# Kernel tuning notes

Measured on AMD Instinct MI355X. Metric: run time of the kernel, lower is better.

The kernel has to match this reference:

```python
import jax, jax.numpy as jnp
import numpy as np

D_MODEL = 1024
HEAD = 64

def setup_inputs() -> dict:
    key = jax.random.key(0)
    ks = jax.random.split(key, 7)
    s = 1.0 / np.sqrt(D_MODEL)
    x = jax.random.normal(ks[0], (4, 2048, D_MODEL), dtype=jnp.float32)
    Wq = jax.random.uniform(ks[1], (D_MODEL, HEAD), jnp.float32, -s, s)
    bq = jax.random.uniform(ks[2], (HEAD,), jnp.float32, -s, s)
    Wk = jax.random.uniform(ks[3], (D_MODEL, HEAD), jnp.float32, -s, s)
    bk = jax.random.uniform(ks[4], (HEAD,), jnp.float32, -s, s)
    Wv = jax.random.uniform(ks[5], (D_MODEL, HEAD), jnp.float32, -s, s)
    bv = jax.random.uniform(ks[6], (HEAD,), jnp.float32, -s, s)
    return {"x": x, "Wq": Wq, "bq": bq, "Wk": Wk, "bk": bk, "Wv": Wv, "bv": bv}

def reference(x, Wq, bq, Wk, bk, Wv, bv):
    # x: [b, s, d]
    q = x @ Wq + bq  # [b, s, h]
    k = x @ Wk + bk
    v = x @ Wv + bv
    scale = 1.0 / jnp.sqrt(jnp.asarray(HEAD, x.dtype))
    scores = jnp.einsum('bqh,bkh->bqk', q, k) * scale  # [b, s, s]
    seq_len = x.shape[1]
    mask = jnp.triu(jnp.ones((seq_len, seq_len), dtype=bool), k=1)
    scores = jnp.where(mask, -jnp.inf, scores)
    attn = jax.nn.softmax(scores, axis=-1)
    return jnp.einsum('bqk,bkh->bqh', attn, v)
```

## Files before the change

kernel.cpp:

```cpp
#include <hip/hip_runtime.h>
#include <hip/hip_bf16.h>

#define D_MODEL 1024
#define HEAD    64
#define SEQ     2048
#define BATCH   4
#define ROWS    (BATCH * SEQ)

typedef __attribute__((ext_vector_type(8))) short  short8;
typedef __attribute__((ext_vector_type(4))) short  short4v;
typedef __attribute__((ext_vector_type(4))) float  f32x4;

__device__ __forceinline__ unsigned short f2bf(float f) {
    union { __hip_bfloat16 h; unsigned short u; } c;
    c.h = __float2bfloat16(f);
    return c.u;
}

__global__ __launch_bounds__(256) void conv_w(
    const float* __restrict__ Wq, const float* __restrict__ Wk,
    const float* __restrict__ Wv, unsigned short* __restrict__ Wt)
{
    __shared__ float Lw[64][65];
    const int tid = threadIdx.x;
    const int mat = blockIdx.x >> 4;
    const int k0  = (blockIdx.x & 15) * 64;
    const float* W = (mat == 0) ? Wq : (mat == 1 ? Wk : Wv);

    #pragma unroll
    for (int j = 0; j < 4; ++j) {
        const int idx = j * 1024 + tid * 4;
        const int r = idx >> 6, c = idx & 63;
        f32x4 v4 = *(const f32x4*)(W + (size_t)(k0 + r) * HEAD + c);
        Lw[r][c] = v4[0]; Lw[r][c+1] = v4[1]; Lw[r][c+2] = v4[2]; Lw[r][c+3] = v4[3];
    }
    __syncthreads();

    const int col = tid >> 2, kc = (tid & 3) * 16;
    short8 o0, o1;
    #pragma unroll
    for (int j = 0; j < 8; ++j) o0[j] = f2bf(Lw[kc + j][col]);
    #pragma unroll
    for (int j = 0; j < 8; ++j) o1[j] = f2bf(Lw[kc + 8 + j][col]);
    unsigned short* dst = Wt + (size_t)(mat * 64 + col) * D_MODEL + k0 + kc;
    *(short8*)(dst)     = o0;
    *(short8*)(dst + 8) = o1;
}

__global__ __launch_bounds__(256) void gemm_qkv(
    const float* __restrict__ x, const unsigned short* __restrict__ Wt,
    const float* __restrict__ bq, const float* __restrict__ bk,
    const float* __restrict__ bv,
    unsigned short* __restrict__ qb, unsigned short* __restrict__ kb,
    unsigned short* __restrict__ vt)
{
    __shared__ unsigned short Xs[16 * 1032];
    __shared__ float Vx[16][66];

    const int tid  = threadIdx.x;
    const int lane = tid & 63;
    const int w    = tid >> 6;
    const int l15  = lane & 15;
    const int g    = lane >> 4;
    const int row0 = blockIdx.x * 16;

    {
        const int xrow  = tid >> 4;
        const int cbase = (tid & 15) * 4;
        #pragma unroll
        for (int j = 0; j < 16; ++j) {
            const int col = j * 64 + cbase;
            f32x4 v4 = *(const f32x4*)(x + (size_t)(row0 + xrow) * D_MODEL + col);
            short4v pk;
            pk[0] = f2bf(v4[0]); pk[1] = f2bf(v4[1]);
            pk[2] = f2bf(v4[2]); pk[3] = f2bf(v4[3]);
            *(short4v*)&Xs[xrow * 1032 + col] = pk;
        }
    }
    __syncthreads();

    f32x4 acc[3] = {};
    const size_t wrow0 = (size_t)(w * 48 + l15) * D_MODEL;

    short8 bA[3][2], bB[3][2];
    #pragma unroll
    for (int ni = 0; ni < 3; ++ni) {
        bA[ni][0] = *(const short8*)(Wt + wrow0 + (size_t)ni * 16 * D_MODEL + g * 8);
        bA[ni][1] = *(const short8*)(Wt + wrow0 + (size_t)ni * 16 * D_MODEL + 32 + g * 8);
    }

    auto gbody = [&](int t, short8 (&bcur)[3][2], short8 (&bnxt)[3][2]) {
        const int k0 = t * 64;
        if (t + 1 < 16) {
            #pragma unroll
            for (int ni = 0; ni < 3; ++ni) {
                const size_t base = wrow0 + (size_t)ni * 16 * D_MODEL + k0 + 64;
                bnxt[ni][0] = *(const short8*)(Wt + base + g * 8);
                bnxt[ni][1] = *(const short8*)(Wt + base + 32 + g * 8);
            }
        }
        short8 af0 = *(const short8*)&Xs[l15 * 1032 + k0 + g * 8];
        short8 af1 = *(const short8*)&Xs[l15 * 1032 + k0 + 32 + g * 8];
        #pragma unroll
        for (int ni = 0; ni < 3; ++ni) {
            acc[ni] = __builtin_amdgcn_mfma_f32_16x16x32_bf16(af0, bcur[ni][0], acc[ni], 0, 0, 0);
            acc[ni] = __builtin_amdgcn_mfma_f32_16x16x32_bf16(af1, bcur[ni][1], acc[ni], 0, 0, 0);
        }
    };

    #pragma unroll 1
    for (int t = 0; t < 16; t += 2) {
        gbody(t,     bA, bB);
        gbody(t + 1, bB, bA);
    }

    #pragma unroll
    for (int ni = 0; ni < 3; ++ni) {
        const int col = w * 48 + ni * 16 + l15;
        const int mat = col >> 6, mc = col & 63;
        const float bias = (mat == 0 ? bq : (mat == 1 ? bk : bv))[mc];
        #pragma unroll
        for (int r = 0; r < 4; ++r) {
            const int rl = g * 4 + r;
            const float val = acc[ni][r] + bias;
            if (mat == 0)      qb[(size_t)(row0 + rl) * HEAD + mc] = f2bf(val * 0.125f);
            else if (mat == 1) kb[(size_t)(row0 + rl) * HEAD + mc] = f2bf(val);
            else               Vx[rl][mc] = val;
        }
    }
    __syncthreads();

    {
        const int d = tid >> 2, kvc = (tid & 3) * 4;
        short4v o;
        #pragma unroll
        for (int j = 0; j < 4; ++j) o[j] = f2bf(Vx[kvc + j][d]);
        const int bb = row0 >> 11, kvloc = row0 & 2047;
        *(short4v*)(vt + ((size_t)bb * HEAD + d) * SEQ + kvloc + kvc) = o;
    }
}

__global__ __launch_bounds__(512) void attn_fwd(
    const unsigned short* __restrict__ qb, const unsigned short* __restrict__ kb,
    const unsigned short* __restrict__ vt, float* __restrict__ out)
{
    __shared__ unsigned short Qs[16 * 68];
    __shared__ unsigned short Ps[8][16 * 40];
    __shared__ float Cs[8][16 * 68];
    __shared__ float Sm[128], Sl[128];

    const int tid  = threadIdx.x;
    const int lane = tid & 63;
    const int w    = tid >> 6;
    const int l15  = lane & 15;
    const int g    = lane >> 4;
    const int b    = blockIdx.y;
    const int p    = blockIdx.x;

    const unsigned short* qg = qb + (size_t)b * SEQ * HEAD;
    const unsigned short* kg = kb + (size_t)b * SEQ * HEAD;
    const unsigned short* vg = vt + (size_t)b * HEAD * SEQ;

    #pragma unroll 1
    for (int half = 0; half < 2; ++half) {
        const int j     = half ? (127 - p) : p;
        const int q0    = j * 16;
        const int iters = (q0 + 16 + 255) >> 8;

        if (tid < 128) {
            const int row = tid >> 3, slot = tid & 7;
            *(short8*)&Qs[row * 68 + slot * 8] =
                *(const short8*)(qg + (size_t)(q0 + row) * HEAD + slot * 8);
        }
        __syncthreads();

        const short8 qf0 = *(const short8*)&Qs[l15 * 68 + g * 8];
        const short8 qf1 = *(const short8*)&Qs[l15 * 68 + 32 + g * 8];

        float m_w = -1.0e30f, l_w = 0.0f;
        f32x4 acc[4] = {};

        short8 kA[4], kB2[4];
        #pragma unroll
        for (int u = 0; u < 4; ++u) {
            const int f = u >> 1, ks = u & 1;
            kA[u] = *(const short8*)(
                kg + (size_t)(w * 32 + f * 16 + l15) * HEAD + ks * 32 + g * 8);
        }

        auto body = [&](int it, short8 (&kcur)[4], short8 (&knxt)[4]) {
            const int kv0 = it * 256;

            short8 vc0, vc1, vc2, vc3;
            {
                const size_t vb = (size_t)l15 * SEQ + kv0 + w * 32 + g * 8;
                vc0 = *(const short8*)(vg + vb);
                vc1 = *(const short8*)(vg + vb + (size_t)16 * SEQ);
                vc2 = *(const short8*)(vg + vb + (size_t)32 * SEQ);
                vc3 = *(const short8*)(vg + vb + (size_t)48 * SEQ);
            }

            if (it + 1 < iters) {
                #pragma unroll
                for (int u = 0; u < 4; ++u) {
                    const int f = u >> 1, ks = u & 1;
                    knxt[u] = *(const short8*)(
                        kg + (size_t)(kv0 + 256 + w * 32 + f * 16 + l15) * HEAD
                           + ks * 32 + g * 8);
                }
            }

            f32x4 sA[2] = {};
            sA[0] = __builtin_amdgcn_mfma_f32_16x16x32_bf16(kcur[0], qf0, sA[0], 0, 0, 0);
            sA[0] = __builtin_amdgcn_mfma_f32_16x16x32_bf16(kcur[1], qf1, sA[0], 0, 0, 0);
            sA[1] = __builtin_amdgcn_mfma_f32_16x16x32_bf16(kcur[2], qf0, sA[1], 0, 0, 0);
            sA[1] = __builtin_amdgcn_mfma_f32_16x16x32_bf16(kcur[3], qf1, sA[1], 0, 0, 0);

            if (it == iters - 1) {
                const int kvb = kv0 + w * 32 + g * 4;
                const int qq  = q0 + l15;
                #pragma unroll
                for (int f = 0; f < 2; ++f)
                    #pragma unroll
                    for (int r = 0; r < 4; ++r)
                        if (kvb + f * 16 + r > qq) sA[f][r] = -1.0e30f;
            }

            float smax = sA[0][0];
            #pragma unroll
            for (int r = 1; r < 4; ++r) smax = fmaxf(smax, sA[0][r]);
            #pragma unroll
            for (int r = 0; r < 4; ++r) smax = fmaxf(smax, sA[1][r]);
            smax = fmaxf(smax, __shfl_xor(smax, 16));
            smax = fmaxf(smax, __shfl_xor(smax, 32));

            const float mnew = fmaxf(m_w, smax);
            const float corr = __expf(m_w - mnew);
            float pv[8], psum = 0.0f;
            #pragma unroll
            for (int f = 0; f < 2; ++f)
                #pragma unroll
                for (int r = 0; r < 4; ++r) {
                    pv[f * 4 + r] = __expf(sA[f][r] - mnew);
                    psum += pv[f * 4 + r];
                }
            psum += __shfl_xor(psum, 16);
            psum += __shfl_xor(psum, 32);
            l_w = l_w * corr + psum;
            m_w = mnew;

            #pragma unroll
            for (int f = 0; f < 2; ++f) {
                short4v pk;
                pk[0] = f2bf(pv[f*4+0]); pk[1] = f2bf(pv[f*4+1]);
                pk[2] = f2bf(pv[f*4+2]); pk[3] = f2bf(pv[f*4+3]);
                *(short4v*)&Ps[w][l15 * 40 + f * 16 + g * 4] = pk;
            }

            float cf[4];
            #pragma unroll
            for (int r = 0; r < 4; ++r) cf[r] = __shfl(corr, g * 4 + r);
            #pragma unroll
            for (int ni = 0; ni < 4; ++ni)
                #pragma unroll
                for (int r = 0; r < 4; ++r) acc[ni][r] *= cf[r];

            const short8 pf = *(const short8*)&Ps[w][l15 * 40 + g * 8];
            acc[0] = __builtin_amdgcn_mfma_f32_16x16x32_bf16(pf, vc0, acc[0], 0, 0, 0);
            acc[1] = __builtin_amdgcn_mfma_f32_16x16x32_bf16(pf, vc1, acc[1], 0, 0, 0);
            acc[2] = __builtin_amdgcn_mfma_f32_16x16x32_bf16(pf, vc2, acc[2], 0, 0, 0);
            acc[3] = __builtin_amdgcn_mfma_f32_16x16x32_bf16(pf, vc3, acc[3], 0, 0, 0);
        };

        #pragma unroll 1
        for (int itp = 0; itp < iters; itp += 2) {
            body(itp, kA, kB2);
            if (itp + 1 < iters) body(itp + 1, kB2, kA);
        }

        if (lane < 16) { Sm[w * 16 + lane] = m_w; Sl[w * 16 + lane] = l_w; }
        #pragma unroll
        for (int ni = 0; ni < 4; ++ni)
            #pragma unroll
            for (int r = 0; r < 4; ++r)
                Cs[w][(g * 4 + r) * 68 + ni * 16 + l15] = acc[ni][r];
        __syncthreads();

        if (tid < 256) {
            const int q = tid >> 4, d4 = (tid & 15) * 4;
            float mg = Sm[q];
            #pragma unroll
            for (int ww = 1; ww < 8; ++ww) mg = fmaxf(mg, Sm[ww * 16 + q]);
            f32x4 o = {0.f, 0.f, 0.f, 0.f};
            float lt = 0.0f;
            #pragma unroll
            for (int ww = 0; ww < 8; ++ww) {
                const float f = __expf(Sm[ww * 16 + q] - mg);
                lt += Sl[ww * 16 + q] * f;
                f32x4 c4 = *(const f32x4*)&Cs[ww][q * 68 + d4];
                o[0] += c4[0] * f; o[1] += c4[1] * f;
                o[2] += c4[2] * f; o[3] += c4[3] * f;
            }
            const float inv = 1.0f / lt;
            f32x4 res = {o[0]*inv, o[1]*inv, o[2]*inv, o[3]*inv};
            *(f32x4*)(out + ((size_t)b * SEQ + q0 + q) * HEAD + d4) = res;
        }
        __syncthreads();
    }
}

extern "C" void kernel_launch(void* const* d_in, const int* in_sizes, int n_in,
                              void* d_out, int out_size, void* d_ws, size_t ws_size,
                              hipStream_t stream) {
    const float* x  = (const float*)d_in[0];
    const float* Wq = (const float*)d_in[1];
    const float* bq = (const float*)d_in[2];
    const float* Wk = (const float*)d_in[3];
    const float* bk = (const float*)d_in[4];
    const float* Wv = (const float*)d_in[5];
    const float* bv = (const float*)d_in[6];

    unsigned short* Wt  = (unsigned short*)d_ws;
    unsigned short* qbp = Wt + (size_t)192 * D_MODEL;
    unsigned short* kbp = qbp + (size_t)ROWS * HEAD;
    unsigned short* vtp = kbp + (size_t)ROWS * HEAD;
    float* o = (float*)d_out;

    conv_w  <<<dim3(48),     dim3(256), 0, stream>>>(Wq, Wk, Wv, Wt);
    gemm_qkv<<<dim3(512),    dim3(256), 0, stream>>>(x, Wt, bq, bk, bv, qbp, kbp, vtp);
    attn_fwd<<<dim3(64, 4),  dim3(512), 0, stream>>>(qbp, kbp, vtp, o);
}
```

Measured before the change: 129.6 us.

## Fuse weight conversion, QKV GEMM and attention into one cooperative kernel

Replaces the three separate launches with a single cooperative kernel of 256 blocks of 512 threads that uses grid-wide syncs between the weight-conversion, QKV projection and attention phases, with shared memory reused through a union. The QKV GEMM now gives each block 32 rows across 8 waves, and the attention loop double-buffers V loads alongside K prefetches. The aim is to remove launch gaps and tail effects between kernels. The cost is grid.sync overhead and only 256 blocks for the GEMM phase.

```diff
diff --git a/kernel.cpp b/kernel.cpp
--- a/kernel.cpp
+++ b/kernel.cpp
@@ -1,5 +1,8 @@
 #include <hip/hip_runtime.h>
 #include <hip/hip_bf16.h>
+#include <hip/hip_cooperative_groups.h>
+
+namespace cg = cooperative_groups;
 
 #define D_MODEL 1024
 #define HEAD    64
@@ -17,54 +20,60 @@
     return c.u;
 }
 
-__global__ __launch_bounds__(256) void conv_w(
-    const float* __restrict__ Wq, const float* __restrict__ Wk,
-    const float* __restrict__ Wv, unsigned short* __restrict__ Wt)
+__global__ __launch_bounds__(512, 2) void fused_all(
+    const float* __restrict__ x,
+    const float* __restrict__ Wq, const float* __restrict__ bq,
+    const float* __restrict__ Wk, const float* __restrict__ bk,
+    const float* __restrict__ Wv, const float* __restrict__ bv,
+    unsigned short* __restrict__ Wt,
+    unsigned short* __restrict__ qb, unsigned short* __restrict__ kb,
+    unsigned short* __restrict__ vt, float* __restrict__ out)
 {
-    __shared__ float Lw[64][65];
-    const int tid = threadIdx.x;
-    const int mat = blockIdx.x >> 4;
-    const int k0  = (blockIdx.x & 15) * 64;
-    const float* W = (mat == 0) ? Wq : (mat == 1 ? Wk : Wv);
-
-    #pragma unroll
-    for (int j = 0; j < 4; ++j) {
-        const int idx = j * 1024 + tid * 4;
-        const int r = idx >> 6, c = idx & 63;
-        f32x4 v4 = *(const f32x4*)(W + (size_t)(k0 + r) * HEAD + c);
-        Lw[r][c] = v4[0]; Lw[r][c+1] = v4[1]; Lw[r][c+2] = v4[2]; Lw[r][c+3] = v4[3];
-    }
-    __syncthreads();
-
-    const int col = tid >> 2, kc = (tid & 3) * 16;
-    short8 o0, o1;
-    #pragma unroll
-    for (int j = 0; j < 8; ++j) o0[j] = f2bf(Lw[kc + j][col]);
-    #pragma unroll
-    for (int j = 0; j < 8; ++j) o1[j] = f2bf(Lw[kc + 8 + j][col]);
-    unsigned short* dst = Wt + (size_t)(mat * 64 + col) * D_MODEL + k0 + kc;
-    *(short8*)(dst)     = o0;
-    *(short8*)(dst + 8) = o1;
-}
-
-__global__ __launch_bounds__(256) void gemm_qkv(
-    const float* __restrict__ x, const unsigned short* __restrict__ Wt,
-    const float* __restrict__ bq, const float* __restrict__ bk,
-    const float* __restrict__ bv,
-    unsigned short* __restrict__ qb, unsigned short* __restrict__ kb,
-    unsigned short* __restrict__ vt)
-{
-    __shared__ unsigned short Xs[16 * 1032];
-    __shared__ float Vx[16][66];
+    __shared__ union SMem {
+        struct { float Lw[64][65]; } a;
+        struct { unsigned short Xs[32 * 1032];
+                 float Vx[32][66]; } bp;
+        struct { unsigned short Qs[16 * 68];
+                 unsigned short Ps[8][16 * 40];
+                 float Cs[8][16 * 68];
+                 float Sm[128], Sl[128]; } c;
+    } sm;
+
+    cg::grid_group grid = cg::this_grid();
 
     const int tid  = threadIdx.x;
+    const int bx   = blockIdx.x;
     const int lane = tid & 63;
     const int w    = tid >> 6;
     const int l15  = lane & 15;
     const int g    = lane >> 4;
-    const int row0 = blockIdx.x * 16;
+
+    if (bx < 48) {
+        const int mat = bx >> 4;
+        const int k0  = (bx & 15) * 64;
+        const float* W = (mat == 0) ? Wq : (mat == 1 ? Wk : Wv);
+        #pragma unroll
+        for (int j = 0; j < 2; ++j) {
+            const int idx = j * 2048 + tid * 4;
+            const int r = idx >> 6, cc = idx & 63;
+            f32x4 v4 = *(const f32x4*)(W + (size_t)(k0 + r) * HEAD + cc);
+            sm.a.Lw[r][cc]   = v4[0]; sm.a.Lw[r][cc+1] = v4[1];
+            sm.a.Lw[r][cc+2] = v4[2]; sm.a.Lw[r][cc+3] = v4[3];
+        }
+        __syncthreads();
+        const int col = tid >> 3, kc = (tid & 7) * 8;
+        short8 o;
+        #pragma unroll
+        for (int j = 0; j < 8; ++j) o[j] = f2bf(sm.a.Lw[kc + j][col]);
+        *(short8*)(Wt + (size_t)(mat * 64 + col) * D_MODEL + k0 + kc) = o;
+    }
+
+    grid.sync();
 
     {
+        const int wr = w & 1, wc = w >> 1;
+        const int row0 = bx * 32;
+
         const int xrow  = tid >> 4;
         const int cbase = (tid & 15) * 4;
         #pragma unroll
@@ -74,238 +83,224 @@
             short4v pk;
             pk[0] = f2bf(v4[0]); pk[1] = f2bf(v4[1]);
             pk[2] = f2bf(v4[2]); pk[3] = f2bf(v4[3]);
-            *(short4v*)&Xs[xrow * 1032 + col] = pk;
+            *(short4v*)&sm.bp.Xs[xrow * 1032 + col] = pk;
+        }
+        __syncthreads();
+
+        f32x4 acc[3] = {};
+        const size_t wrow0 = (size_t)(wc * 48 + l15) * D_MODEL;
+
+        short8 bA[3][2], bB[3][2];
+        #pragma unroll
+        for (int ni = 0; ni < 3; ++ni) {
+            const size_t base = wrow0 + (size_t)ni * 16 * D_MODEL;
+            bA[ni][0] = *(const short8*)(Wt + base + g * 8);
+            bA[ni][1] = *(const short8*)(Wt + base + 32 + g * 8);
+        }
+
+        auto gbody = [&](int t, short8 (&bcur)[3][2], short8 (&bnxt)[3][2]) {
+            const int k0 = t * 64;
+            if (t + 1 < 16) {
+                #pragma unroll
+                for (int ni = 0; ni < 3; ++ni) {
+                    const size_t base = wrow0 + (size_t)ni * 16 * D_MODEL + k0 + 64;
+                    bnxt[ni][0] = *(const short8*)(Wt + base + g * 8);
+                    bnxt[ni][1] = *(const short8*)(Wt + base + 32 + g * 8);
+                }
+            }
+            short8 af0 = *(const short8*)&sm.bp.Xs[(wr * 16 + l15) * 1032 + k0 + g * 8];
+            short8 af1 = *(const short8*)&sm.bp.Xs[(wr * 16 + l15) * 1032 + k0 + 32 + g * 8];
+            #pragma unroll
+            for (int ni = 0; ni < 3; ++ni) {
+                acc[ni] = __builtin_amdgcn_mfma_f32_16x16x32_bf16(af0, bcur[ni][0], acc[ni], 0, 0, 0);
+                acc[ni] = __builtin_amdgcn_mfma_f32_16x16x32_bf16(af1, bcur[ni][1], acc[ni], 0, 0, 0);
+            }
+        };
+
+        #pragma unroll 1
+        for (int t = 0; t < 16; t += 2) {
+            gbody(t,     bA, bB);
+            gbody(t + 1, bB, bA);
+        }
+
+        #pragma unroll
+        for (int ni = 0; ni < 3; ++ni) {
+            const int col = wc * 48 + ni * 16 + l15;
+            const int mat = col >> 6, mc = col & 63;
+            const float bias = (mat == 0 ? bq : (mat == 1 ? bk : bv))[mc];
+            #pragma unroll
+            for (int r = 0; r < 4; ++r) {
+                const int rl = wr * 16 + g * 4 + r;
+                const float val = acc[ni][r] + bias;
+                if (mat == 0)      qb[(size_t)(row0 + rl) * HEAD + mc] = f2bf(val * 0.125f);
+                else if (mat == 1) kb[(size_t)(row0 + rl) * HEAD + mc] = f2bf(val);
+                else               sm.bp.Vx[rl][mc] = val;
+            }
+        }
+        __syncthreads();
+
+        {
+            const int d = tid >> 3, kvc = (tid & 7) * 4;
+            short4v o;
+            #pragma unroll
+            for (int j = 0; j < 4; ++j) o[j] = f2bf(sm.bp.Vx[kvc + j][d]);
+            const int bb = row0 >> 11, kvloc = row0 & 2047;
+            *(short4v*)(vt + ((size_t)bb * HEAD + d) * SEQ + kvloc + kvc) = o;
         }
     }
-    __syncthreads();
-
-    f32x4 acc[3] = {};
-    const size_t wrow0 = (size_t)(w * 48 + l15) * D_MODEL;
-
-    short8 bA[3][2], bB[3][2];
-    #pragma unroll
-    for (int ni = 0; ni < 3; ++ni) {
-        bA[ni][0] = *(const short8*)(Wt + wrow0 + (size_t)ni * 16 * D_MODEL + g * 8);
-        bA[ni][1] = *(const short8*)(Wt + wrow0 + (size_t)ni * 16 * D_MODEL + 32 + g * 8);
-    }
-
-    auto gbody = [&](int t, short8 (&bcur)[3][2], short8 (&bnxt)[3][2]) {
-        const int k0 = t * 64;
-        if (t + 1 < 16) {
-            #pragma unroll
-            for (int ni = 0; ni < 3; ++ni) {
-                const size_t base = wrow0 + (size_t)ni * 16 * D_MODEL + k0 + 64;
-                bnxt[ni][0] = *(const short8*)(Wt + base + g * 8);
-                bnxt[ni][1] = *(const short8*)(Wt + base + 32 + g * 8);
-            }
-        }
-        short8 af0 = *(const short8*)&Xs[l15 * 1032 + k0 + g * 8];
-        short8 af1 = *(const short8*)&Xs[l15 * 1032 + k0 + 32 + g * 8];
-        #pragma unroll
-        for (int ni = 0; ni < 3; ++ni) {
-            acc[ni] = __builtin_amdgcn_mfma_f32_16x16x32_bf16(af0, bcur[ni][0], acc[ni], 0, 0, 0);
-            acc[ni] = __builtin_amdgcn_mfma_f32_16x16x32_bf16(af1, bcur[ni][1], acc[ni], 0, 0, 0);
-        }
-    };
-
-    #pragma unroll 1
-    for (int t = 0; t < 16; t += 2) {
-        gbody(t,     bA, bB);
-        gbody(t + 1, bB, bA);
-    }
-
-    #pragma unroll
-    for (int ni = 0; ni < 3; ++ni) {
-        const int col = w * 48 + ni * 16 + l15;
-        const int mat = col >> 6, mc = col & 63;
-        const float bias = (mat == 0 ? bq : (mat == 1 ? bk : bv))[mc];
-        #pragma unroll
-        for (int r = 0; r < 4; ++r) {
-            const int rl = g * 4 + r;
-            const float val = acc[ni][r] + bias;
-            if (mat == 0)      qb[(size_t)(row0 + rl) * HEAD + mc] = f2bf(val * 0.125f);
-            else if (mat == 1) kb[(size_t)(row0 + rl) * HEAD + mc] = f2bf(val);
-            else               Vx[rl][mc] = val;
-        }
-    }
-    __syncthreads();
+
+    grid.sync();
 
     {
-        const int d = tid >> 2, kvc = (tid & 3) * 4;
-        short4v o;
-        #pragma unroll
-        for (int j = 0; j < 4; ++j) o[j] = f2bf(Vx[kvc + j][d]);
-        const int bb = row0 >> 11, kvloc = row0 & 2047;
-        *(short4v*)(vt + ((size_t)bb * HEAD + d) * SEQ + kvloc + kvc) = o;
-    }
-}
-
-__global__ __launch_bounds__(512) void attn_fwd(
-    const unsigned short* __restrict__ qb, const unsigned short* __restrict__ kb,
-    const unsigned short* __restrict__ vt, float* __restrict__ out)
-{
-    __shared__ unsigned short Qs[16 * 68];
-    __shared__ unsigned short Ps[8][16 * 40];
-    __shared__ float Cs[8][16 * 68];
-    __shared__ float Sm[128], Sl[128];
-
-    const int tid  = threadIdx.x;
-    const int lane = tid & 63;
-    const int w    = tid >> 6;
-    const int l15  = lane & 15;
-    const int g    = lane >> 4;
-    const int b    = blockIdx.y;
-    const int p    = blockIdx.x;
-
-    const unsigned short* qg = qb + (size_t)b * SEQ * HEAD;
-    const unsigned short* kg = kb + (size_t)b * SEQ * HEAD;
-    const unsigned short* vg = vt + (size_t)b * HEAD * SEQ;
-
-    #pragma unroll 1
-    for (int half = 0; half < 2; ++half) {
-        const int j     = half ? (127 - p) : p;
-        const int q0    = j * 16;
-        const int iters = (q0 + 16 + 255) >> 8;
-
-        if (tid < 128) {
-            const int row = tid >> 3, slot = tid & 7;
-            *(short8*)&Qs[row * 68 + slot * 8] =
-                *(const short8*)(qg + (size_t)(q0 + row) * HEAD + slot * 8);
-        }
-        __syncthreads();
-
-        const short8 qf0 = *(const short8*)&Qs[l15 * 68 + g * 8];
-        const short8 qf1 = *(const short8*)&Qs[l15 * 68 + 32 + g * 8];
-
-        float m_w = -1.0e30f, l_w = 0.0f;
-        f32x4 acc[4] = {};
-
-        short8 kA[4], kB2[4];
-        #pragma unroll
-        for (int u = 0; u < 4; ++u) {
-            const int f = u >> 1, ks = u & 1;
-            kA[u] = *(const short8*)(
-                kg + (size_t)(w * 32 + f * 16 + l15) * HEAD + ks * 32 + g * 8);
-        }
-
-        auto body = [&](int it, short8 (&kcur)[4], short8 (&knxt)[4]) {
-            const int kv0 = it * 256;
-
-            short8 vc0, vc1, vc2, vc3;
-            {
-                const size_t vb = (size_t)l15 * SEQ + kv0 + w * 32 + g * 8;
-                vc0 = *(const short8*)(vg + vb);
-                vc1 = *(const short8*)(vg + vb + (size_t)16 * SEQ);
-                vc2 = *(const short8*)(vg + vb + (size_t)32 * SEQ);
-                vc3 = *(const short8*)(vg + vb + (size_t)48 * SEQ);
-            }
-
-            if (it + 1 < iters) {
-                #pragma unroll
-                for (int u = 0; u < 4; ++u) {
-                    const int f = u >> 1, ks = u & 1;
-                    knxt[u] = *(const short8*)(
-                        kg + (size_t)(kv0 + 256 + w * 32 + f * 16 + l15) * HEAD
-                           + ks * 32 + g * 8);
-                }
-            }
-
-            f32x4 sA[2] = {};
-            sA[0] = __builtin_amdgcn_mfma_f32_16x16x32_bf16(kcur[0], qf0, sA[0], 0, 0, 0);
-            sA[0] = __builtin_amdgcn_mfma_f32_16x16x32_bf16(kcur[1], qf1, sA[0], 0, 0, 0);
-            sA[1] = __builtin_amdgcn_mfma_f32_16x16x32_bf16(kcur[2], qf0, sA[1], 0, 0, 0);
-            sA[1] = __builtin_amdgcn_mfma_f32_16x16x32_bf16(kcur[3], qf1, sA[1], 0, 0, 0);
-
-            if (it == iters - 1) {
-                const int kvb = kv0 + w * 32 + g * 4;
-                const int qq  = q0 + l15;
+        const int b = bx >> 6;
+        const int p = bx & 63;
+
+        const unsigned short* qg = qb + (size_t)b * SEQ * HEAD;
+        const unsigned short* kg = kb + (size_t)b * SEQ * HEAD;
+        const unsigned short* vg = vt + (size_t)b * HEAD * SEQ;
+
+        #pragma unroll 1
+        for (int half = 0; half < 2; ++half) {
+            const int j     = half ? (127 - p) : p;
+            const int q0    = j * 16;
+            const int iters = (q0 + 16 + 255) >> 8;
+
+            if (tid < 128) {
+                const int row = tid >> 3, slot = tid & 7;
+                *(short8*)&sm.c.Qs[row * 68 + slot * 8] =
+                    *(const short8*)(qg + (size_t)(q0 + row) * HEAD + slot * 8);
+            }
+            __syncthreads();
+
+            const short8 qf0 = *(const short8*)&sm.c.Qs[l15 * 68 + g * 8];
+            const short8 qf1 = *(const short8*)&sm.c.Qs[l15 * 68 + 32 + g * 8];
+
+            float m_w = -1.0e30f, l_w = 0.0f;
+            f32x4 acc[4] = {};
+
+            short8 kA[4], kB2[4], vA[4], vB[4];
+            #pragma unroll
+            for (int u = 0; u < 4; ++u) {
+                const int f = u >> 1, ks = u & 1;
+                kA[u] = *(const short8*)(
+                    kg + (size_t)(w * 32 + f * 16 + l15) * HEAD + ks * 32 + g * 8);
+                vA[u] = *(const short8*)(
+                    vg + (size_t)(u * 16 + l15) * SEQ + w * 32 + g * 8);
+            }
+
+            auto body = [&](int it, short8 (&kcur)[4], short8 (&knxt)[4],
+                                    short8 (&vcur)[4], short8 (&vnxt)[4]) {
+                const int kv0 = it * 256;
+
+                if (it + 1 < iters) {
+                    #pragma unroll
+                    for (int u = 0; u < 4; ++u) {
+                        const int f = u >> 1, ks = u & 1;
+                        knxt[u] = *(const short8*)(
+                            kg + (size_t)(kv0 + 256 + w * 32 + f * 16 + l15) * HEAD
+                               + ks * 32 + g * 8);
+                        vnxt[u] = *(const short8*)(
+                            vg + (size_t)(u * 16 + l15) * SEQ + kv0 + 256 + w * 32 + g * 8);
+                    }
+                }
+
+                f32x4 sA[2] = {};
+                sA[0] = __builtin_amdgcn_mfma_f32_16x16x32_bf16(kcur[0], qf0, sA[0], 0, 0, 0);
+                sA[0] = __builtin_amdgcn_mfma_f32_16x16x32_bf16(kcur[1], qf1, sA[0], 0, 0, 0);
+                sA[1] = __builtin_amdgcn_mfma_f32_16x16x32_bf16(kcur[2], qf0, sA[1], 0, 0, 0);
+                sA[1] = __builtin_amdgcn_mfma_f32_16x16x32_bf16(kcur[3], qf1, sA[1], 0, 0, 0);
+
+                if (it == iters - 1) {
+                    const int kvb = kv0 + w * 32 + g * 4;
+                    const int qq  = q0 + l15;
+                    #pragma unroll
+                    for (int f = 0; f < 2; ++f)
+                        #pragma unroll
+                        for (int r = 0; r < 4; ++r)
+                            if (kvb + f * 16 + r > qq) sA[f][r] = -1.0e30f;
+                }
+
+                float smax = sA[0][0];
+                #pragma unroll
+                for (int r = 1; r < 4; ++r) smax = fmaxf(smax, sA[0][r]);
+                #pragma unroll
+                for (int r = 0; r < 4; ++r) smax = fmaxf(smax, sA[1][r]);
+                smax = fmaxf(smax, __shfl_xor(smax, 16));
+                smax = fmaxf(smax, __shfl_xor(smax, 32));
+
+                const float mnew = fmaxf(m_w, smax);
+                const float corr = __expf(m_w - mnew);
+                float pv[8], psum = 0.0f;
                 #pragma unroll
                 for (int f = 0; f < 2; ++f)
                     #pragma unroll
-                    for (int r = 0; r < 4; ++r)
-                        if (kvb + f * 16 + r > qq) sA[f][r] = -1.0e30f;
-            }
-
-            float smax = sA[0][0];
-            #pragma unroll
-            for (int r = 1; r < 4; ++r) smax = fmaxf(smax, sA[0][r]);
-            #pragma unroll
-            for (int r = 0; r < 4; ++r) smax = fmaxf(smax, sA[1][r]);
-            smax = fmaxf(smax, __shfl_xor(smax, 16));
-            smax = fmaxf(smax, __shfl_xor(smax, 32));
-
-            const float mnew = fmaxf(m_w, smax);
-            const float corr = __expf(m_w - mnew);
-            float pv[8], psum = 0.0f;
-            #pragma unroll
-            for (int f = 0; f < 2; ++f)
-                #pragma unroll
-                for (int r = 0; r < 4; ++r) {
-                    pv[f * 4 + r] = __expf(sA[f][r] - mnew);
-                    psum += pv[f * 4 + r];
-                }
-            psum += __shfl_xor(psum, 16);
-            psum += __shfl_xor(psum, 32);
-            l_w = l_w * corr + psum;
-            m_w = mnew;
-
-            #pragma unroll
-            for (int f = 0; f < 2; ++f) {
-                short4v pk;
-                pk[0] = f2bf(pv[f*4+0]); pk[1] = f2bf(pv[f*4+1]);
-                pk[2] = f2bf(pv[f*4+2]); pk[3] = f2bf(pv[f*4+3]);
-                *(short4v*)&Ps[w][l15 * 40 + f * 16 + g * 4] = pk;
-            }
-
-            float cf[4];
-            #pragma unroll
-            for (int r = 0; r < 4; ++r) cf[r] = __shfl(corr, g * 4 + r);
+                    for (int r = 0; r < 4; ++r) {
+                        pv[f * 4 + r] = __expf(sA[f][r] - mnew);
+                        psum += pv[f * 4 + r];
+                    }
+                psum += __shfl_xor(psum, 16);
+                psum += __shfl_xor(psum, 32);
+                l_w = l_w * corr + psum;
+                m_w = mnew;
+
+                #pragma unroll
+                for (int f = 0; f < 2; ++f) {
+                    short4v pk;
+                    pk[0] = f2bf(pv[f*4+0]); pk[1] = f2bf(pv[f*4+1]);
+                    pk[2] = f2bf(pv[f*4+2]); pk[3] = f2bf(pv[f*4+3]);
+                    *(short4v*)&sm.c.Ps[w][l15 * 40 + f * 16 + g * 4] = pk;
+                }
+
+                float cf[4];
+                #pragma unroll
+                for (int r = 0; r < 4; ++r) cf[r] = __shfl(corr, g * 4 + r);
+                #pragma unroll
+                for (int ni = 0; ni < 4; ++ni)
+                    #pragma unroll
+                    for (int r = 0; r < 4; ++r) acc[ni][r] *= cf[r];
+
+                const short8 pf = *(const short8*)&sm.c.Ps[w][l15 * 40 + g * 8];
+                acc[0] = __builtin_amdgcn_mfma_f32_16x16x32_bf16(pf, vcur[0], acc[0], 0, 0, 0);
+                acc[1] = __builtin_amdgcn_mfma_f32_16x16x32_bf16(pf, vcur[1], acc[1], 0, 0, 0);
+                acc[2] = __builtin_amdgcn_mfma_f32_16x16x32_bf16(pf, vcur[2], acc[2], 0, 0, 0);
+                acc[3] = __builtin_amdgcn_mfma_f32_16x16x32_bf16(pf, vcur[3], acc[3], 0, 0, 0);
+            };
+
+            #pragma unroll 1
+            for (int itp = 0; itp < iters; itp += 2) {
+                body(itp, kA, kB2, vA, vB);
+                if (itp + 1 < iters) body(itp + 1, kB2, kA, vB, vA);
+            }
+
+            if (lane < 16) { sm.c.Sm[w * 16 + lane] = m_w; sm.c.Sl[w * 16 + lane] = l_w; }
             #pragma unroll
             for (int ni = 0; ni < 4; ++ni)
                 #pragma unroll
-                for (int r = 0; r < 4; ++r) acc[ni][r] *= cf[r];
-
-            const short8 pf = *(const short8*)&Ps[w][l15 * 40 + g * 8];
-            acc[0] = __builtin_amdgcn_mfma_f32_16x16x32_bf16(pf, vc0, acc[0], 0, 0, 0);
-            acc[1] = __builtin_amdgcn_mfma_f32_16x16x32_bf16(pf, vc1, acc[1], 0, 0, 0);
-            acc[2] = __builtin_amdgcn_mfma_f32_16x16x32_bf16(pf, vc2, acc[2], 0, 0, 0);
-            acc[3] = __builtin_amdgcn_mfma_f32_16x16x32_bf16(pf, vc3, acc[3], 0, 0, 0);
-        };
-
-        #pragma unroll 1
-        for (int itp = 0; itp < iters; itp += 2) {
-            body(itp, kA, kB2);
-            if (itp + 1 < iters) body(itp + 1, kB2, kA);
-        }
-
-        if (lane < 16) { Sm[w * 16 + lane] = m_w; Sl[w * 16 + lane] = l_w; }
-        #pragma unroll
-        for (int ni = 0; ni < 4; ++ni)
-            #pragma unroll
-            for (int r = 0; r < 4; ++r)
-                Cs[w][(g * 4 + r) * 68 + ni * 16 + l15] = acc[ni][r];
-        __syncthreads();
-
-        if (tid < 256) {
-            const int q = tid >> 4, d4 = (tid & 15) * 4;
-            float mg = Sm[q];
-            #pragma unroll
-            for (int ww = 1; ww < 8; ++ww) mg = fmaxf(mg, Sm[ww * 16 + q]);
-            f32x4 o = {0.f, 0.f, 0.f, 0.f};
-            float lt = 0.0f;
-            #pragma unroll
-            for (int ww = 0; ww < 8; ++ww) {
-                const float f = __expf(Sm[ww * 16 + q] - mg);
-                lt += Sl[ww * 16 + q] * f;
-                f32x4 c4 = *(const f32x4*)&Cs[ww][q * 68 + d4];
-                o[0] += c4[0] * f; o[1] += c4[1] * f;
-                o[2] += c4[2] * f; o[3] += c4[3] * f;
-            }
-            const float inv = 1.0f / lt;
-            f32x4 res = {o[0]*inv, o[1]*inv, o[2]*inv, o[3]*inv};
-            *(f32x4*)(out + ((size_t)b * SEQ + q0 + q) * HEAD + d4) = res;
-        }
-        __syncthreads();
+                for (int r = 0; r < 4; ++r)
+                    sm.c.Cs[w][(g * 4 + r) * 68 + ni * 16 + l15] = acc[ni][r];
+            __syncthreads();
+
+            if (tid < 256) {
+                const int q = tid >> 4, d4 = (tid & 15) * 4;
+                float mg = sm.c.Sm[q];
+                #pragma unroll
+                for (int ww = 1; ww < 8; ++ww) mg = fmaxf(mg, sm.c.Sm[ww * 16 + q]);
+                f32x4 o = {0.f, 0.f, 0.f, 0.f};
+                float lt = 0.0f;
+                #pragma unroll
+                for (int ww = 0; ww < 8; ++ww) {
+                    const float f = __expf(sm.c.Sm[ww * 16 + q] - mg);
+                    lt += sm.c.Sl[ww * 16 + q] * f;
+                    f32x4 c4 = *(const f32x4*)&sm.c.Cs[ww][q * 68 + d4];
+                    o[0] += c4[0] * f; o[1] += c4[1] * f;
+                    o[2] += c4[2] * f; o[3] += c4[3] * f;
+                }
+                const float inv = 1.0f / lt;
+                f32x4 res = {o[0]*inv, o[1]*inv, o[2]*inv, o[3]*inv};
+                *(f32x4*)(out + ((size_t)b * SEQ + q0 + q) * HEAD + d4) = res;
+            }
+            __syncthreads();
+        }
     }
 }
 
@@ -326,7 +321,9 @@
     unsigned short* vtp = kbp + (size_t)ROWS * HEAD;
     float* o = (float*)d_out;
 
-    conv_w  <<<dim3(48),     dim3(256), 0, stream>>>(Wq, Wk, Wv, Wt);
-    gemm_qkv<<<dim3(512),    dim3(256), 0, stream>>>(x, Wt, bq, bk, bv, qbp, kbp, vtp);
-    attn_fwd<<<dim3(64, 4),  dim3(512), 0, stream>>>(qbp, kbp, vtp, o);
+    void* args[] = { (void*)&x, (void*)&Wq, (void*)&bq, (void*)&Wk, (void*)&bk,
+                     (void*)&Wv, (void*)&bv, (void*)&Wt, (void*)&qbp, (void*)&kbp,
+                     (void*)&vtp, (void*)&o };
+    hipLaunchCooperativeKernel((const void*)fused_all, dim3(256), dim3(512),
+                               args, 0, stream);
 }
```

New measurement: 198.3 us. 53.0% more time.

## Split causal attention KV range across blocks with separate partial-softmax reduce kernel

Applied to the files above, without the earlier changes.

Replaces the paired-query-tile attention kernel with a split-KV scheme: each 16-query tile's causal KV range is divided into 512-wide chunks, each handled by its own 256-thread block, giving 1280 blocks instead of 256. Partial outputs with row max and sum are written to workspace and merged by a new reduce kernel, while tiles needing a single chunk write the output directly. The PV MFMA operand order is swapped so the correction factor no longer needs cross-lane shuffles. The aim is better CU occupancy and load balance, at the cost of an extra launch and workspace traffic.

```diff
diff --git a/kernel.cpp b/kernel.cpp
--- a/kernel.cpp
+++ b/kernel.cpp
@@ -140,173 +140,209 @@
     }
 }
 
-__global__ __launch_bounds__(512) void attn_fwd(
+__global__ __launch_bounds__(256, 4) void attn_part(
     const unsigned short* __restrict__ qb, const unsigned short* __restrict__ kb,
-    const unsigned short* __restrict__ vt, float* __restrict__ out)
+    const unsigned short* __restrict__ vt, float* __restrict__ out,
+    float* __restrict__ pws)
 {
     __shared__ unsigned short Qs[16 * 68];
-    __shared__ unsigned short Ps[8][16 * 40];
-    __shared__ float Cs[8][16 * 68];
-    __shared__ float Sm[128], Sl[128];
+    __shared__ unsigned short Ps[4][16 * 40];
+    __shared__ float Cs[4][16 * 68];
+    __shared__ float Sm[64], Sl[64];
 
     const int tid  = threadIdx.x;
     const int lane = tid & 63;
     const int w    = tid >> 6;
     const int l15  = lane & 15;
     const int g    = lane >> 4;
+    const int t    = blockIdx.x;
     const int b    = blockIdx.y;
-    const int p    = blockIdx.x;
+
+    int j, c, nch;
+    if (t < 32)       { j = t;                  c = 0;             nch = 1; }
+    else if (t < 96)  { int u = t - 32;  j = 32 + (u >> 1); c = u & 1;         nch = 2; }
+    else if (t < 192) { int u = t - 96;  j = 64 + u / 3;    c = u - (u / 3) * 3; nch = 3; }
+    else              { int u = t - 192; j = 96 + (u >> 2); c = u & 3;         nch = 4; }
+
+    const int q0    = j * 16;
+    const int kv_lo = c * 512;
+    const int kv_hi = min(kv_lo + 512, q0 + 16);
 
     const unsigned short* qg = qb + (size_t)b * SEQ * HEAD;
     const unsigned short* kg = kb + (size_t)b * SEQ * HEAD;
     const unsigned short* vg = vt + (size_t)b * HEAD * SEQ;
 
-    #pragma unroll 1
-    for (int half = 0; half < 2; ++half) {
-        const int j     = half ? (127 - p) : p;
-        const int q0    = j * 16;
-        const int iters = (q0 + 16 + 255) >> 8;
-
-        if (tid < 128) {
-            const int row = tid >> 3, slot = tid & 7;
-            *(short8*)&Qs[row * 68 + slot * 8] =
-                *(const short8*)(qg + (size_t)(q0 + row) * HEAD + slot * 8);
-        }
-        __syncthreads();
-
-        const short8 qf0 = *(const short8*)&Qs[l15 * 68 + g * 8];
-        const short8 qf1 = *(const short8*)&Qs[l15 * 68 + 32 + g * 8];
-
-        float m_w = -1.0e30f, l_w = 0.0f;
-        f32x4 acc[4] = {};
-
+    if (tid < 128) {
+        const int row = tid >> 3, slot = tid & 7;
+        *(short8*)&Qs[row * 68 + slot * 8] =
+            *(const short8*)(qg + (size_t)(q0 + row) * HEAD + slot * 8);
+    }
+    __syncthreads();
+
+    const short8 qf0 = *(const short8*)&Qs[l15 * 68 + g * 8];
+    const short8 qf1 = *(const short8*)&Qs[l15 * 68 + 32 + g * 8];
+
+    float m_w = -1.0e30f, l_w = 0.0f;
+    f32x4 acc[4] = {};
+
+    const int lo_w = kv_lo + w * 32;
+    const int ns   = (kv_hi > lo_w) ? min(4, (kv_hi - lo_w + 127) >> 7) : 0;
+    const int qq   = q0 + l15;
+
+    auto body = [&](int s, short8 (&kcur)[4], short8 (&knxt)[4]) {
+        const int kv0 = lo_w + s * 128;
+
+        short8 vc0, vc1, vc2, vc3;
+        {
+            const size_t vbs = (size_t)l15 * SEQ + kv0 + g * 8;
+            vc0 = *(const short8*)(vg + vbs);
+            vc1 = *(const short8*)(vg + vbs + (size_t)16 * SEQ);
+            vc2 = *(const short8*)(vg + vbs + (size_t)32 * SEQ);
+            vc3 = *(const short8*)(vg + vbs + (size_t)48 * SEQ);
+        }
+
+        if (s + 1 < ns) {
+            #pragma unroll
+            for (int u = 0; u < 4; ++u) {
+                const int f = u >> 1, ks = u & 1;
+                knxt[u] = *(const short8*)(
+                    kg + (size_t)(kv0 + 128 + f * 16 + l15) * HEAD + ks * 32 + g * 8);
+            }
+        }
+
+        f32x4 sA[2] = {};
+        sA[0] = __builtin_amdgcn_mfma_f32_16x16x32_bf16(kcur[0], qf0, sA[0], 0, 0, 0);
+        sA[0] = __builtin_amdgcn_mfma_f32_16x16x32_bf16(kcur[1], qf1, sA[0], 0, 0, 0);
+        sA[1] = __builtin_amdgcn_mfma_f32_16x16x32_bf16(kcur[2], qf0, sA[1], 0, 0, 0);
+        sA[1] = __builtin_amdgcn_mfma_f32_16x16x32_bf16(kcur[3], qf1, sA[1], 0, 0, 0);
+
+        if (kv0 + 32 > q0) {
+            const int kvb = kv0 + g * 4;
+            #pragma unroll
+            for (int f = 0; f < 2; ++f)
+                #pragma unroll
+                for (int r = 0; r < 4; ++r)
+                    if (kvb + f * 16 + r > qq) sA[f][r] = -1.0e30f;
+        }
+
+        float smax = sA[0][0];
+        #pragma unroll
+        for (int r = 1; r < 4; ++r) smax = fmaxf(smax, sA[0][r]);
+        #pragma unroll
+        for (int r = 0; r < 4; ++r) smax = fmaxf(smax, sA[1][r]);
+        smax = fmaxf(smax, __shfl_xor(smax, 16));
+        smax = fmaxf(smax, __shfl_xor(smax, 32));
+
+        const float mnew = fmaxf(m_w, smax);
+        const float corr = __expf(m_w - mnew);
+        float pv[8], psum = 0.0f;
+        #pragma unroll
+        for (int f = 0; f < 2; ++f)
+            #pragma unroll
+            for (int r = 0; r < 4; ++r) {
+                pv[f * 4 + r] = __expf(sA[f][r] - mnew);
+                psum += pv[f * 4 + r];
+            }
+        psum += __shfl_xor(psum, 16);
+        psum += __shfl_xor(psum, 32);
+        l_w = l_w * corr + psum;
+        m_w = mnew;
+
+        #pragma unroll
+        for (int f = 0; f < 2; ++f) {
+            short4v pk;
+            pk[0] = f2bf(pv[f*4+0]); pk[1] = f2bf(pv[f*4+1]);
+            pk[2] = f2bf(pv[f*4+2]); pk[3] = f2bf(pv[f*4+3]);
+            *(short4v*)&Ps[w][l15 * 40 + f * 16 + g * 4] = pk;
+        }
+
+        #pragma unroll
+        for (int ni = 0; ni < 4; ++ni)
+            #pragma unroll
+            for (int r = 0; r < 4; ++r) acc[ni][r] *= corr;
+
+        const short8 pf = *(const short8*)&Ps[w][l15 * 40 + g * 8];
+        acc[0] = __builtin_amdgcn_mfma_f32_16x16x32_bf16(vc0, pf, acc[0], 0, 0, 0);
+        acc[1] = __builtin_amdgcn_mfma_f32_16x16x32_bf16(vc1, pf, acc[1], 0, 0, 0);
+        acc[2] = __builtin_amdgcn_mfma_f32_16x16x32_bf16(vc2, pf, acc[2], 0, 0, 0);
+        acc[3] = __builtin_amdgcn_mfma_f32_16x16x32_bf16(vc3, pf, acc[3], 0, 0, 0);
+    };
+
+    if (ns > 0) {
         short8 kA[4], kB2[4];
         #pragma unroll
         for (int u = 0; u < 4; ++u) {
             const int f = u >> 1, ks = u & 1;
             kA[u] = *(const short8*)(
-                kg + (size_t)(w * 32 + f * 16 + l15) * HEAD + ks * 32 + g * 8);
-        }
-
-        auto body = [&](int it, short8 (&kcur)[4], short8 (&knxt)[4]) {
-            const int kv0 = it * 256;
-
-            short8 vc0, vc1, vc2, vc3;
-            {
-                const size_t vb = (size_t)l15 * SEQ + kv0 + w * 32 + g * 8;
-                vc0 = *(const short8*)(vg + vb);
-                vc1 = *(const short8*)(vg + vb + (size_t)16 * SEQ);
-                vc2 = *(const short8*)(vg + vb + (size_t)32 * SEQ);
-                vc3 = *(const short8*)(vg + vb + (size_t)48 * SEQ);
-            }
-
-            if (it + 1 < iters) {
-                #pragma unroll
-                for (int u = 0; u < 4; ++u) {
-                    const int f = u >> 1, ks = u & 1;
-                    knxt[u] = *(const short8*)(
-                        kg + (size_t)(kv0 + 256 + w * 32 + f * 16 + l15) * HEAD
-                           + ks * 32 + g * 8);
-                }
-            }
-
-            f32x4 sA[2] = {};
-            sA[0] = __builtin_amdgcn_mfma_f32_16x16x32_bf16(kcur[0], qf0, sA[0], 0, 0, 0);
-            sA[0] = __builtin_amdgcn_mfma_f32_16x16x32_bf16(kcur[1], qf1, sA[0], 0, 0, 0);
-            sA[1] = __builtin_amdgcn_mfma_f32_16x16x32_bf16(kcur[2], qf0, sA[1], 0, 0, 0);
-            sA[1] = __builtin_amdgcn_mfma_f32_16x16x32_bf16(kcur[3], qf1, sA[1], 0, 0, 0);
-
-            if (it == iters - 1) {
-                const int kvb = kv0 + w * 32 + g * 4;
-                const int qq  = q0 + l15;
-                #pragma unroll
-                for (int f = 0; f < 2; ++f)
-                    #pragma unroll
-                    for (int r = 0; r < 4; ++r)
-                        if (kvb + f * 16 + r > qq) sA[f][r] = -1.0e30f;
-            }
-
-            float smax = sA[0][0];
-            #pragma unroll
-            for (int r = 1; r < 4; ++r) smax = fmaxf(smax, sA[0][r]);
-            #pragma unroll
-            for (int r = 0; r < 4; ++r) smax = fmaxf(smax, sA[1][r]);
-            smax = fmaxf(smax, __shfl_xor(smax, 16));
-            smax = fmaxf(smax, __shfl_xor(smax, 32));
-
-            const float mnew = fmaxf(m_w, smax);
-            const float corr = __expf(m_w - mnew);
-            float pv[8], psum = 0.0f;
-            #pragma unroll
-            for (int f = 0; f < 2; ++f)
-                #pragma unroll
-                for (int r = 0; r < 4; ++r) {
-                    pv[f * 4 + r] = __expf(sA[f][r] - mnew);
-                    psum += pv[f * 4 + r];
-                }
-            psum += __shfl_xor(psum, 16);
-            psum += __shfl_xor(psum, 32);
-            l_w = l_w * corr + psum;
-            m_w = mnew;
-
-            #pragma unroll
-            for (int f = 0; f < 2; ++f) {
-                short4v pk;
-                pk[0] = f2bf(pv[f*4+0]); pk[1] = f2bf(pv[f*4+1]);
-                pk[2] = f2bf(pv[f*4+2]); pk[3] = f2bf(pv[f*4+3]);
-                *(short4v*)&Ps[w][l15 * 40 + f * 16 + g * 4] = pk;
-            }
-
-            float cf[4];
-            #pragma unroll
-            for (int r = 0; r < 4; ++r) cf[r] = __shfl(corr, g * 4 + r);
-            #pragma unroll
-            for (int ni = 0; ni < 4; ++ni)
-                #pragma unroll
-                for (int r = 0; r < 4; ++r) acc[ni][r] *= cf[r];
-
-            const short8 pf = *(const short8*)&Ps[w][l15 * 40 + g * 8];
-            acc[0] = __builtin_amdgcn_mfma_f32_16x16x32_bf16(pf, vc0, acc[0], 0, 0, 0);
-            acc[1] = __builtin_amdgcn_mfma_f32_16x16x32_bf16(pf, vc1, acc[1], 0, 0, 0);
-            acc[2] = __builtin_amdgcn_mfma_f32_16x16x32_bf16(pf, vc2, acc[2], 0, 0, 0);
-            acc[3] = __builtin_amdgcn_mfma_f32_16x16x32_bf16(pf, vc3, acc[3], 0, 0, 0);
-        };
-
-        #pragma unroll 1
-        for (int itp = 0; itp < iters; itp += 2) {
-            body(itp, kA, kB2);
-            if (itp + 1 < iters) body(itp + 1, kB2, kA);
-        }
-
-        if (lane < 16) { Sm[w * 16 + lane] = m_w; Sl[w * 16 + lane] = l_w; }
-        #pragma unroll
-        for (int ni = 0; ni < 4; ++ni)
-            #pragma unroll
-            for (int r = 0; r < 4; ++r)
-                Cs[w][(g * 4 + r) * 68 + ni * 16 + l15] = acc[ni][r];
-        __syncthreads();
-
-        if (tid < 256) {
-            const int q = tid >> 4, d4 = (tid & 15) * 4;
-            float mg = Sm[q];
-            #pragma unroll
-            for (int ww = 1; ww < 8; ++ww) mg = fmaxf(mg, Sm[ww * 16 + q]);
-            f32x4 o = {0.f, 0.f, 0.f, 0.f};
-            float lt = 0.0f;
-            #pragma unroll
-            for (int ww = 0; ww < 8; ++ww) {
-                const float f = __expf(Sm[ww * 16 + q] - mg);
-                lt += Sl[ww * 16 + q] * f;
-                f32x4 c4 = *(const f32x4*)&Cs[ww][q * 68 + d4];
-                o[0] += c4[0] * f; o[1] += c4[1] * f;
-                o[2] += c4[2] * f; o[3] += c4[3] * f;
-            }
+                kg + (size_t)(lo_w + f * 16 + l15) * HEAD + ks * 32 + g * 8);
+        }
+        body(0, kA, kB2);
+        if (ns > 1) body(1, kB2, kA);
+        if (ns > 2) body(2, kA, kB2);
+        if (ns > 3) body(3, kB2, kA);
+    }
+
+    if (lane < 16) { Sm[w * 16 + lane] = m_w; Sl[w * 16 + lane] = l_w; }
+    #pragma unroll
+    for (int ni = 0; ni < 4; ++ni)
+        *(f32x4*)&Cs[w][l15 * 68 + ni * 16 + g * 4] = acc[ni];
+    __syncthreads();
+
+    {
+        const int q = tid >> 4, d4 = (tid & 15) * 4;
+        float mg = Sm[q];
+        #pragma unroll
+        for (int ww = 1; ww < 4; ++ww) mg = fmaxf(mg, Sm[ww * 16 + q]);
+        f32x4 o = {0.f, 0.f, 0.f, 0.f};
+        float lt = 0.0f;
+        #pragma unroll
+        for (int ww = 0; ww < 4; ++ww) {
+            const float f = __expf(Sm[ww * 16 + q] - mg);
+            lt += Sl[ww * 16 + q] * f;
+            f32x4 c4 = *(const f32x4*)&Cs[ww][q * 68 + d4];
+            o[0] += c4[0] * f; o[1] += c4[1] * f;
+            o[2] += c4[2] * f; o[3] += c4[3] * f;
+        }
+        if (nch == 1) {
             const float inv = 1.0f / lt;
             f32x4 res = {o[0]*inv, o[1]*inv, o[2]*inv, o[3]*inv};
             *(f32x4*)(out + ((size_t)b * SEQ + q0 + q) * HEAD + d4) = res;
-        }
-        __syncthreads();
-    }
+        } else {
+            float* pp = pws + (size_t)((b * 128 + j) * 4 + c) * 1056;
+            *(f32x4*)(pp + q * 64 + d4) = o;
+            if ((tid & 15) == 0) { pp[1024 + q] = mg; pp[1040 + q] = lt; }
+        }
+    }
+}
+
+__global__ __launch_bounds__(256) void attn_reduce(
+    const float* __restrict__ pws, float* __restrict__ out)
+{
+    const int jj  = 32 + blockIdx.x;
+    const int b   = blockIdx.y;
+    const int nch = (jj >> 5) + 1;
+    const int q   = threadIdx.x >> 4;
+    const int d4  = (threadIdx.x & 15) * 4;
+
+    const float* p0 = pws + (size_t)((b * 128 + jj) * 4) * 1056;
+
+    float mg = -1.0e30f;
+    for (int cc = 0; cc < nch; ++cc)
+        mg = fmaxf(mg, p0[(size_t)cc * 1056 + 1024 + q]);
+
+    f32x4 o = {0.f, 0.f, 0.f, 0.f};
+    float lt = 0.0f;
+    for (int cc = 0; cc < nch; ++cc) {
+        const float* pc = p0 + (size_t)cc * 1056;
+        const float f = __expf(pc[1024 + q] - mg);
+        lt += pc[1040 + q] * f;
+        f32x4 a4 = *(const f32x4*)(pc + q * 64 + d4);
+        o[0] += a4[0] * f; o[1] += a4[1] * f;
+        o[2] += a4[2] * f; o[3] += a4[3] * f;
+    }
+    const float inv = 1.0f / lt;
+    f32x4 res = {o[0]*inv, o[1]*inv, o[2]*inv, o[3]*inv};
+    *(f32x4*)(out + ((size_t)b * SEQ + jj * 16 + q) * HEAD + d4) = res;
 }
 
 extern "C" void kernel_launch(void* const* d_in, const int* in_sizes, int n_in,
@@ -324,9 +360,11 @@
     unsigned short* qbp = Wt + (size_t)192 * D_MODEL;
     unsigned short* kbp = qbp + (size_t)ROWS * HEAD;
     unsigned short* vtp = kbp + (size_t)ROWS * HEAD;
+    float*          pws = (float*)(vtp + (size_t)ROWS * HEAD);
     float* o = (float*)d_out;
 
-    conv_w  <<<dim3(48),     dim3(256), 0, stream>>>(Wq, Wk, Wv, Wt);
-    gemm_qkv<<<dim3(512),    dim3(256), 0, stream>>>(x, Wt, bq, bk, bv, qbp, kbp, vtp);
-    attn_fwd<<<dim3(64, 4),  dim3(512), 0, stream>>>(qbp, kbp, vtp, o);
-}
+    conv_w     <<<dim3(48),       dim3(256), 0, stream>>>(Wq, Wk, Wv, Wt);
+    gemm_qkv   <<<dim3(512),      dim3(256), 0, stream>>>(x, Wt, bq, bk, bv, qbp, kbp, vtp);
+    attn_part  <<<dim3(320, 4),   dim3(256), 0, stream>>>(qbp, kbp, vtp, o, pws);
+    attn_reduce<<<dim3(96, 4),    dim3(256), 0, stream>>>(pws, o);
+}
```

Result: slower. 134.0 us (+3.4%).
